# Kernel optimization log

Hardware: AMD Instinct MI355X
Metric: run time of the kernel (lower is better)

## Reference

```python
import jax, jax.numpy as jnp
import numpy as np
from jax import lax

NUM_GROUP = 512
GROUP_SIZE = 32


def setup_inputs() -> dict:
    key = jax.random.key(0)
    xyz = jax.random.normal(key, (8, 8192, 6), dtype=jnp.float32)
    return {"xyz": xyz}


def _fps_indices(pts, K):
    """Farthest point sampling. pts: [B,N,3] -> idx [B,K] int32. Start at point 0."""
    B, N, _ = pts.shape
    first = jnp.zeros((B,), dtype=jnp.int32)
    # squared distance of every point to the first selected point
    d = jnp.sum((pts - pts[:, :1, :]) ** 2, axis=-1)  # [B,N]

    def step(d, _):
        nxt = jnp.argmax(d, axis=1).astype(jnp.int32)              # [B]
        newp = jnp.take_along_axis(pts, nxt[:, None, None], axis=1)  # [B,1,3]
        d = jnp.minimum(d, jnp.sum((pts - newp) ** 2, axis=-1))
        return d, nxt

    _, rest = lax.scan(step, d, None, length=K - 1)  # rest: [K-1,B]
    idx = jnp.concatenate([first[None, :], rest], axis=0)  # [K,B]
    return idx.T  # [B,K]


def _group(xyz, num_group, group_size):
    coords = xyz[:, :, :3]    # [B,N,3]
    normals = xyz[:, :, 3:6]  # [B,N,3]

    fps_idx = _fps_indices(coords, num_group)                          # [B,G]
    center = jnp.take_along_axis(coords, fps_idx[:, :, None], axis=1)  # [B,G,3]

    # pairwise squared distances center->points: [B,G,N]
    c2 = jnp.sum(center ** 2, axis=-1)[:, :, None]
    x2 = jnp.sum(coords ** 2, axis=-1)[:, None, :]
    cx = jnp.einsum('bgd,bnd->bgn', center, coords)
    d2 = c2 - 2.0 * cx + x2

    _, knn_idx = lax.top_k(-d2, group_size)  # [B,G,M] nearest neighbors

    flat_idx = knn_idx.reshape(knn_idx.shape[0], -1)  # [B,G*M]
    neigh = jnp.take_along_axis(coords, flat_idx[:, :, None], axis=1)
    neigh = neigh.reshape(-1, num_group, group_size, 3) - center[:, :, None, :]
    neigh_n = jnp.take_along_axis(normals, flat_idx[:, :, None], axis=1)
    neigh_n = neigh_n.reshape(-1, num_group, group_size, 3)
    return neigh, neigh_n, center


def reference(xyz):
    return _group(xyz, NUM_GROUP, GROUP_SIZE)
```

## Files before the change

### kernel.cpp

```cpp
#include <hip/hip_runtime.h>
#include <stdint.h>

#define BATCH 8
#define NPTS 8192
#define NGRP 512
#define GSZ 32

typedef float vf2 __attribute__((ext_vector_type(2)));

__device__ __forceinline__ float sq3(float dx, float dy, float dz) {
    return __fadd_rn(__fadd_rn(__fmul_rn(dx, dx), __fmul_rn(dy, dy)), __fmul_rn(dz, dz));
}

template <int C>
__device__ __forceinline__ float dpp_max_f32_step(float v) {
    const int t = __builtin_amdgcn_update_dpp(__float_as_int(v), __float_as_int(v),
                                              C, 0xF, 0xF, false);
    return fmaxf(v, __int_as_float(t));
}
template <int C>
__device__ __forceinline__ unsigned dpp_min_u32_step(unsigned v) {
    const unsigned t = (unsigned)__builtin_amdgcn_update_dpp((int)v, (int)v,
                                                             C, 0xF, 0xF, false);
    return v < t ? v : t;
}
__device__ __forceinline__ float wave_max_f32(float v) {
    v = dpp_max_f32_step<0x111>(v);
    v = dpp_max_f32_step<0x112>(v);
    v = dpp_max_f32_step<0x114>(v);
    v = dpp_max_f32_step<0x118>(v);
    v = dpp_max_f32_step<0x142>(v);
    v = dpp_max_f32_step<0x143>(v);
    return __int_as_float(__builtin_amdgcn_readlane(__float_as_int(v), 63));
}
__device__ __forceinline__ unsigned wave_min_u32(unsigned v) {
    v = dpp_min_u32_step<0x111>(v);
    v = dpp_min_u32_step<0x112>(v);
    v = dpp_min_u32_step<0x114>(v);
    v = dpp_min_u32_step<0x118>(v);
    v = dpp_min_u32_step<0x142>(v);
    v = dpp_min_u32_step<0x143>(v);
    return (unsigned)__builtin_amdgcn_readlane((int)v, 63);
}

__global__ __launch_bounds__(512) void fps_kernel(const float* __restrict__ xyz,
                                                  float* __restrict__ centers) {
    const int b = blockIdx.x;
    const int tid = threadIdx.x;
    const int wv = tid >> 6;

    __shared__ float4 P4[NPTS];
    __shared__ double pkey[2][8];
    __shared__ float cl[NGRP * 3];

    vf2 px[8], py[8], pz[8], d2[8];
    const float* base = xyz + (size_t)b * NPTS * 6;

#pragma unroll
    for (int i = 0; i < 16; ++i) {
        const int p = i * 512 + tid;
        const float4 v4 = *reinterpret_cast<const float4*>(base + (size_t)p * 6);
        px[i >> 1][i & 1] = v4.x; py[i >> 1][i & 1] = v4.y; pz[i >> 1][i & 1] = v4.z;
        d2[i >> 1][i & 1] = __int_as_float(0x7f800000);
        P4[p] = make_float4(v4.x, v4.y, v4.z, 0.0f);
    }
    float Bx = base[0], By = base[1], Bz = base[2];
    if (tid == 0) { cl[0] = Bx; cl[1] = By; cl[2] = Bz; }
    __syncthreads();

    for (int k = 1; k < NGRP; ++k) {
        {
#pragma clang fp contract(off)
            const vf2 bx2 = {Bx, Bx}, by2 = {By, By}, bz2 = {Bz, Bz};
#pragma unroll
            for (int j = 0; j < 8; ++j) {
                const vf2 dx = px[j] - bx2;
                const vf2 dy = py[j] - by2;
                const vf2 dz = pz[j] - bz2;
                const vf2 mx2 = dx * dx;
                const vf2 my2 = dy * dy;
                const vf2 mz2 = dz * dz;
                const vf2 s = (mx2 + my2) + mz2;
                d2[j] = __builtin_elementwise_min(d2[j], s);
            }
        }
        vf2 mv = d2[0];
#pragma unroll
        for (int j = 1; j < 8; ++j) mv = __builtin_elementwise_max(mv, d2[j]);
        const float mx = fmaxf(mv[0], mv[1]);
        const float wmx = wave_max_f32(mx);
        int wi = 0;
#pragma unroll
        for (int i = 15; i >= 1; --i) {
            wi = (d2[i >> 1][i & 1] == mx) ? i : wi;
        }
        unsigned widx_w;
        const unsigned long long bal = __ballot(mx == wmx);
        if (__popcll(bal) == 1) {
            const int L = __ffsll(bal) - 1;
            widx_w = (unsigned)(__builtin_amdgcn_readlane(wi, L) * 512 + (wv * 64 + L));
        } else {
            const unsigned cand = (mx == wmx) ? (unsigned)(wi * 512 + tid) : 0xFFFFFFFFu;
            widx_w = wave_min_u32(cand);
        }

        const int buf = k & 1;
        if ((tid & 63) == 0) {
            pkey[buf][wv] = __hiloint2double(__float_as_int(wmx), 8191 - (int)widx_w);
        }
        __syncthreads();

        const double2* pp = reinterpret_cast<const double2*>(&pkey[buf][0]);
        const double2 a = pp[0], c = pp[1], e = pp[2], f = pp[3];
        const double g = fmax(fmax(fmax(a.x, a.y), fmax(c.x, c.y)),
                              fmax(fmax(e.x, e.y), fmax(f.x, f.y)));
        const int widx = 8191 - __double2loint(g);
        const float4 c4 = P4[widx];
        Bx = c4.x; By = c4.y; Bz = c4.z;

        if (tid == 0) { cl[k * 3 + 0] = Bx; cl[k * 3 + 1] = By; cl[k * 3 + 2] = Bz; }
    }

    __syncthreads();
    float* cg = centers + (size_t)b * NGRP * 3;
    for (int t = tid; t < NGRP * 3; t += 512) cg[t] = cl[t];
}

__global__ __launch_bounds__(256) void knn_kernel(const float* __restrict__ xyz,
                                                  const float* __restrict__ centers,
                                                  float* __restrict__ neigh,
                                                  float* __restrict__ neigh_n) {
    const int row = blockIdx.x;
    const int b = row >> 9;
    const int tid = threadIdx.x;
    const int lane = tid & 63;
    const int wv = tid >> 6;

    __shared__ unsigned long long rk[2][4];
    __shared__ int sel[GSZ];

    const float* cptr = centers + (size_t)row * 3;
    const float cx = cptr[0], cy = cptr[1], cz = cptr[2];
    const float c2 = sq3(cx, cy, cz);

    const float* base = xyz + (size_t)b * NPTS * 6;
    unsigned long long key[32];
#pragma unroll
    for (int i = 0; i < 32; ++i) {
        const int p = i * 256 + tid;
        const float4 v4 = *reinterpret_cast<const float4*>(base + (size_t)p * 6);
        const float x = v4.x, y = v4.y, z = v4.z;
        const float x2 = sq3(x, y, z);
        const float dot = __fmaf_rn(cz, z, __fmaf_rn(cy, y, __fmul_rn(cx, x)));
        const float d2 = __fadd_rn(__fsub_rn(c2, __fmul_rn(2.0f, dot)), x2);
        unsigned u = __float_as_uint(d2);
        u ^= (unsigned)(((int)u >> 31)) | 0x80000000u;
        key[i] = ((unsigned long long)u << 32) | (unsigned)p;
    }

    unsigned long long lm = ~0ULL, lm2v = ~0ULL;
#pragma unroll
    for (int i = 0; i < 32; ++i) {
        const unsigned long long kk = key[i];
        const bool a = kk < lm;
        const bool b2 = kk < lm2v;
        lm2v = a ? lm : (b2 ? kk : lm2v);
        lm = a ? kk : lm;
    }

    for (int r = 0; r < GSZ; ++r) {
        const unsigned hi = (unsigned)(lm >> 32);
        const unsigned minhi = wave_min_u32(hi);
        unsigned minlo;
        const unsigned long long bal = __ballot(hi == minhi);
        if (__popcll(bal) == 1) {
            const int L = __ffsll(bal) - 1;
            minlo = (unsigned)__builtin_amdgcn_readlane((int)(unsigned)lm, L);
        } else {
            const unsigned cand = (hi == minhi) ? (unsigned)lm : 0xFFFFFFFFu;
            minlo = wave_min_u32(cand);
        }
        const unsigned long long mk = ((unsigned long long)minhi << 32) | minlo;

        const int rb = r & 1;
        if (lane == 0) rk[rb][wv] = mk;
        __syncthreads();
        const ulonglong2* rp = reinterpret_cast<const ulonglong2*>(&rk[rb][0]);
        const ulonglong2 r0 = rp[0], r1 = rp[1];
        const unsigned long long g01 = r0.x < r0.y ? r0.x : r0.y;
        const unsigned long long g23 = r1.x < r1.y ? r1.x : r1.y;
        const unsigned long long gm = g01 < g23 ? g01 : g23;
        if (tid == 0) sel[r] = (int)(unsigned)(gm & 0xffffffffu);
        if (lm == gm) {
            if (lm2v != 0ULL) {
                lm = lm2v;
            } else {
                unsigned long long nm = ~0ULL;
#pragma unroll
                for (int i = 0; i < 32; ++i) {
                    const unsigned long long v = key[i] > gm ? key[i] : ~0ULL;
                    nm = v < nm ? v : nm;
                }
                lm = nm;
            }
            lm2v = 0ULL;
        }
    }
    __syncthreads();

    if (tid < GSZ) {
        const int idx = sel[tid];
        const float* q = base + (size_t)idx * 6;
        const float4 a4 = *reinterpret_cast<const float4*>(q);
        const float2 b2v = *reinterpret_cast<const float2*>(q + 4);
        const size_t o = ((size_t)row * GSZ + tid) * 3;
        neigh[o + 0] = __fsub_rn(a4.x, cx);
        neigh[o + 1] = __fsub_rn(a4.y, cy);
        neigh[o + 2] = __fsub_rn(a4.z, cz);
        neigh_n[o + 0] = a4.w;
        neigh_n[o + 1] = b2v.x;
        neigh_n[o + 2] = b2v.y;
    }
}

extern "C" void kernel_launch(void* const* d_in, const int* in_sizes, int n_in,
                              void* d_out, int out_size, void* d_ws, size_t ws_size,
                              hipStream_t stream) {
    const float* xyz = (const float*)d_in[0];
    float* out = (float*)d_out;
    float* neigh   = out;
    float* neigh_n = out + (size_t)BATCH * NGRP * GSZ * 3;
    float* centers = out + (size_t)2 * BATCH * NGRP * GSZ * 3;

    fps_kernel<<<BATCH, 512, 0, stream>>>(xyz, centers);
    knn_kernel<<<BATCH * NGRP, 256, 0, stream>>>(xyz, centers, neigh, neigh_n);
}
```

Baseline: 511.9 us.

## Fuse FPS and KNN into a persistent kernel with flag-based streaming of centers

Merges the FPS and KNN kernels into one launch. Eight blocks run farthest point sampling and publish centers in chunks of 16 through workspace arrays and a per-batch release counter. The remaining 248 worker blocks spin on that counter and run KNN for each center as soon as it is available, so KNN overlaps the serial FPS instead of waiting for it to finish. KNN blocks grow to 512 threads with 16 keys per thread. The change relies on all FPS blocks being co-resident with the spinning workers and adds a small zeroing kernel; the workers' spinning and memory traffic may slow the FPS blocks.

After: 547.9 us. +7.0%, slower.

```diff
diff --git a/kernel.cpp b/kernel.cpp
--- a/kernel.cpp
+++ b/kernel.cpp
@@ -5,7 +5,9 @@
 #define NPTS 8192
 #define NGRP 512
 #define GSZ 32
-
+#define NWORK 248
+#define CHUNK 16
+typedef unsigned long long u64;
 typedef float vf2 __attribute__((ext_vector_type(2)));
 
 __device__ __forceinline__ float sq3(float dx, float dy, float dz) {
@@ -43,183 +45,225 @@
     return (unsigned)__builtin_amdgcn_readlane((int)v, 63);
 }
 
-__global__ __launch_bounds__(512) void fps_kernel(const float* __restrict__ xyz,
-                                                  float* __restrict__ centers) {
-    const int b = blockIdx.x;
-    const int tid = threadIdx.x;
-    const int wv = tid >> 6;
-
+__global__ void zero_rc(unsigned* __restrict__ rc) {
+    if (threadIdx.x < BATCH) rc[threadIdx.x] = 0;
+}
+
+__global__ __launch_bounds__(512) void fused_kernel(const float* __restrict__ xyz,
+                                                    float* __restrict__ centers,
+                                                    float* __restrict__ neigh,
+                                                    float* __restrict__ neigh_n,
+                                                    unsigned* __restrict__ rc,
+                                                    unsigned* __restrict__ cpx,
+                                                    unsigned* __restrict__ cpy,
+                                                    unsigned* __restrict__ cpz) {
     __shared__ float4 P4[NPTS];
     __shared__ double pkey[2][8];
     __shared__ float cl[NGRP * 3];
-
-    vf2 px[8], py[8], pz[8], d2[8];
-    const float* base = xyz + (size_t)b * NPTS * 6;
-
-#pragma unroll
-    for (int i = 0; i < 16; ++i) {
-        const int p = i * 512 + tid;
-        const float4 v4 = *reinterpret_cast<const float4*>(base + (size_t)p * 6);
-        px[i >> 1][i & 1] = v4.x; py[i >> 1][i & 1] = v4.y; pz[i >> 1][i & 1] = v4.z;
-        d2[i >> 1][i & 1] = __int_as_float(0x7f800000);
-        P4[p] = make_float4(v4.x, v4.y, v4.z, 0.0f);
-    }
-    float Bx = base[0], By = base[1], Bz = base[2];
-    if (tid == 0) { cl[0] = Bx; cl[1] = By; cl[2] = Bz; }
-    __syncthreads();
-
-    for (int k = 1; k < NGRP; ++k) {
-        {
-#pragma clang fp contract(off)
-            const vf2 bx2 = {Bx, Bx}, by2 = {By, By}, bz2 = {Bz, Bz};
-#pragma unroll
-            for (int j = 0; j < 8; ++j) {
-                const vf2 dx = px[j] - bx2;
-                const vf2 dy = py[j] - by2;
-                const vf2 dz = pz[j] - bz2;
-                const vf2 mx2 = dx * dx;
-                const vf2 my2 = dy * dy;
-                const vf2 mz2 = dz * dz;
-                const vf2 s = (mx2 + my2) + mz2;
-                d2[j] = __builtin_elementwise_min(d2[j], s);
-            }
-        }
-        vf2 mv = d2[0];
-#pragma unroll
-        for (int j = 1; j < 8; ++j) mv = __builtin_elementwise_max(mv, d2[j]);
-        const float mx = fmaxf(mv[0], mv[1]);
-        const float wmx = wave_max_f32(mx);
-        int wi = 0;
-#pragma unroll
-        for (int i = 15; i >= 1; --i) {
-            wi = (d2[i >> 1][i & 1] == mx) ? i : wi;
-        }
-        unsigned widx_w;
-        const unsigned long long bal = __ballot(mx == wmx);
-        if (__popcll(bal) == 1) {
-            const int L = __ffsll(bal) - 1;
-            widx_w = (unsigned)(__builtin_amdgcn_readlane(wi, L) * 512 + (wv * 64 + L));
-        } else {
-            const unsigned cand = (mx == wmx) ? (unsigned)(wi * 512 + tid) : 0xFFFFFFFFu;
-            widx_w = wave_min_u32(cand);
-        }
-
-        const int buf = k & 1;
-        if ((tid & 63) == 0) {
-            pkey[buf][wv] = __hiloint2double(__float_as_int(wmx), 8191 - (int)widx_w);
-        }
-        __syncthreads();
-
-        const double2* pp = reinterpret_cast<const double2*>(&pkey[buf][0]);
-        const double2 a = pp[0], c = pp[1], e = pp[2], f = pp[3];
-        const double g = fmax(fmax(fmax(a.x, a.y), fmax(c.x, c.y)),
-                              fmax(fmax(e.x, e.y), fmax(f.x, f.y)));
-        const int widx = 8191 - __double2loint(g);
-        const float4 c4 = P4[widx];
-        Bx = c4.x; By = c4.y; Bz = c4.z;
-
-        if (tid == 0) { cl[k * 3 + 0] = Bx; cl[k * 3 + 1] = By; cl[k * 3 + 2] = Bz; }
-    }
-
-    __syncthreads();
-    float* cg = centers + (size_t)b * NGRP * 3;
-    for (int t = tid; t < NGRP * 3; t += 512) cg[t] = cl[t];
-}
-
-__global__ __launch_bounds__(256) void knn_kernel(const float* __restrict__ xyz,
-                                                  const float* __restrict__ centers,
-                                                  float* __restrict__ neigh,
-                                                  float* __restrict__ neigh_n) {
-    const int row = blockIdx.x;
-    const int b = row >> 9;
+    __shared__ u64 rk[2][8];
+    __shared__ int sel[GSZ];
+
+    const int wid = blockIdx.x;
     const int tid = threadIdx.x;
     const int lane = tid & 63;
     const int wv = tid >> 6;
 
-    __shared__ unsigned long long rk[2][4];
-    __shared__ int sel[GSZ];
-
-    const float* cptr = centers + (size_t)row * 3;
-    const float cx = cptr[0], cy = cptr[1], cz = cptr[2];
-    const float c2 = sq3(cx, cy, cz);
-
-    const float* base = xyz + (size_t)b * NPTS * 6;
-    unsigned long long key[32];
-#pragma unroll
-    for (int i = 0; i < 32; ++i) {
-        const int p = i * 256 + tid;
-        const float4 v4 = *reinterpret_cast<const float4*>(base + (size_t)p * 6);
-        const float x = v4.x, y = v4.y, z = v4.z;
-        const float x2 = sq3(x, y, z);
-        const float dot = __fmaf_rn(cz, z, __fmaf_rn(cy, y, __fmul_rn(cx, x)));
-        const float d2 = __fadd_rn(__fsub_rn(c2, __fmul_rn(2.0f, dot)), x2);
-        unsigned u = __float_as_uint(d2);
-        u ^= (unsigned)(((int)u >> 31)) | 0x80000000u;
-        key[i] = ((unsigned long long)u << 32) | (unsigned)p;
-    }
-
-    unsigned long long lm = ~0ULL, lm2v = ~0ULL;
-#pragma unroll
-    for (int i = 0; i < 32; ++i) {
-        const unsigned long long kk = key[i];
-        const bool a = kk < lm;
-        const bool b2 = kk < lm2v;
-        lm2v = a ? lm : (b2 ? kk : lm2v);
-        lm = a ? kk : lm;
-    }
-
-    for (int r = 0; r < GSZ; ++r) {
-        const unsigned hi = (unsigned)(lm >> 32);
-        const unsigned minhi = wave_min_u32(hi);
-        unsigned minlo;
-        const unsigned long long bal = __ballot(hi == minhi);
-        if (__popcll(bal) == 1) {
-            const int L = __ffsll(bal) - 1;
-            minlo = (unsigned)__builtin_amdgcn_readlane((int)(unsigned)lm, L);
-        } else {
-            const unsigned cand = (hi == minhi) ? (unsigned)lm : 0xFFFFFFFFu;
-            minlo = wave_min_u32(cand);
+    if (wid < BATCH) {
+        const int b = wid;
+        vf2 px[8], py[8], pz[8], d2[8];
+        const float* base = xyz + (size_t)b * NPTS * 6;
+
+#pragma unroll
+        for (int i = 0; i < 16; ++i) {
+            const int p = i * 512 + tid;
+            const float4 v4 = *reinterpret_cast<const float4*>(base + (size_t)p * 6);
+            px[i >> 1][i & 1] = v4.x; py[i >> 1][i & 1] = v4.y; pz[i >> 1][i & 1] = v4.z;
+            d2[i >> 1][i & 1] = __int_as_float(0x7f800000);
+            P4[p] = make_float4(v4.x, v4.y, v4.z, 0.0f);
         }
-        const unsigned long long mk = ((unsigned long long)minhi << 32) | minlo;
-
-        const int rb = r & 1;
-        if (lane == 0) rk[rb][wv] = mk;
+        float Bx = base[0], By = base[1], Bz = base[2];
+        if (tid == 0) { cl[0] = Bx; cl[1] = By; cl[2] = Bz; }
         __syncthreads();
-        const ulonglong2* rp = reinterpret_cast<const ulonglong2*>(&rk[rb][0]);
-        const ulonglong2 r0 = rp[0], r1 = rp[1];
-        const unsigned long long g01 = r0.x < r0.y ? r0.x : r0.y;
-        const unsigned long long g23 = r1.x < r1.y ? r1.x : r1.y;
-        const unsigned long long gm = g01 < g23 ? g01 : g23;
-        if (tid == 0) sel[r] = (int)(unsigned)(gm & 0xffffffffu);
-        if (lm == gm) {
-            if (lm2v != 0ULL) {
-                lm = lm2v;
+
+        for (int k = 1; k < NGRP; ++k) {
+            {
+#pragma clang fp contract(off)
+                const vf2 bx2 = {Bx, Bx}, by2 = {By, By}, bz2 = {Bz, Bz};
+#pragma unroll
+                for (int j = 0; j < 8; ++j) {
+                    const vf2 dx = px[j] - bx2;
+                    const vf2 dy = py[j] - by2;
+                    const vf2 dz = pz[j] - bz2;
+                    const vf2 mx2 = dx * dx;
+                    const vf2 my2 = dy * dy;
+                    const vf2 mz2 = dz * dz;
+                    const vf2 s = (mx2 + my2) + mz2;
+                    d2[j] = __builtin_elementwise_min(d2[j], s);
+                }
+            }
+            vf2 mv = d2[0];
+#pragma unroll
+            for (int j = 1; j < 8; ++j) mv = __builtin_elementwise_max(mv, d2[j]);
+            const float mx = fmaxf(mv[0], mv[1]);
+            const float wmx = wave_max_f32(mx);
+            int wi = 0;
+#pragma unroll
+            for (int i = 15; i >= 1; --i) {
+                wi = (d2[i >> 1][i & 1] == mx) ? i : wi;
+            }
+            unsigned widx_w;
+            const u64 bal = __ballot(mx == wmx);
+            if (__popcll(bal) == 1) {
+                const int L = __ffsll(bal) - 1;
+                widx_w = (unsigned)(__builtin_amdgcn_readlane(wi, L) * 512 + (wv * 64 + L));
             } else {
-                unsigned long long nm = ~0ULL;
-#pragma unroll
-                for (int i = 0; i < 32; ++i) {
-                    const unsigned long long v = key[i] > gm ? key[i] : ~0ULL;
-                    nm = v < nm ? v : nm;
-                }
-                lm = nm;
-            }
-            lm2v = 0ULL;
+                const unsigned cand = (mx == wmx) ? (unsigned)(wi * 512 + tid) : 0xFFFFFFFFu;
+                widx_w = wave_min_u32(cand);
+            }
+
+            const int buf = k & 1;
+            if ((tid & 63) == 0) {
+                pkey[buf][wv] = __hiloint2double(__float_as_int(wmx), 8191 - (int)widx_w);
+            }
+            __syncthreads();
+
+            const double2* pp = reinterpret_cast<const double2*>(&pkey[buf][0]);
+            const double2 a = pp[0], c = pp[1], e = pp[2], f = pp[3];
+            const double g = fmax(fmax(fmax(a.x, a.y), fmax(c.x, c.y)),
+                                  fmax(fmax(e.x, e.y), fmax(f.x, f.y)));
+            const int widx = 8191 - __double2loint(g);
+            const float4 c4 = P4[widx];
+            Bx = c4.x; By = c4.y; Bz = c4.z;
+
+            if (tid == 0) {
+                cl[k * 3 + 0] = Bx; cl[k * 3 + 1] = By; cl[k * 3 + 2] = Bz;
+                if ((k & (CHUNK - 1)) == (CHUNK - 1)) {
+                    const int k0 = k - (CHUNK - 1);
+#pragma unroll
+                    for (int j = 0; j < CHUNK; ++j) {
+                        const int kk = k0 + j;
+                        const int gi = b * NGRP + kk;
+                        __hip_atomic_store(&cpx[gi], __float_as_uint(cl[kk * 3 + 0]),
+                                           __ATOMIC_RELAXED, __HIP_MEMORY_SCOPE_AGENT);
+                        __hip_atomic_store(&cpy[gi], __float_as_uint(cl[kk * 3 + 1]),
+                                           __ATOMIC_RELAXED, __HIP_MEMORY_SCOPE_AGENT);
+                        __hip_atomic_store(&cpz[gi], __float_as_uint(cl[kk * 3 + 2]),
+                                           __ATOMIC_RELAXED, __HIP_MEMORY_SCOPE_AGENT);
+                    }
+                    __hip_atomic_store(&rc[b], (unsigned)(k + 1),
+                                       __ATOMIC_RELEASE, __HIP_MEMORY_SCOPE_AGENT);
+                }
+            }
         }
-    }
-    __syncthreads();
-
-    if (tid < GSZ) {
-        const int idx = sel[tid];
-        const float* q = base + (size_t)idx * 6;
-        const float4 a4 = *reinterpret_cast<const float4*>(q);
-        const float2 b2v = *reinterpret_cast<const float2*>(q + 4);
-        const size_t o = ((size_t)row * GSZ + tid) * 3;
-        neigh[o + 0] = __fsub_rn(a4.x, cx);
-        neigh[o + 1] = __fsub_rn(a4.y, cy);
-        neigh[o + 2] = __fsub_rn(a4.z, cz);
-        neigh_n[o + 0] = a4.w;
-        neigh_n[o + 1] = b2v.x;
-        neigh_n[o + 2] = b2v.y;
+
+        __syncthreads();
+        float* cg = centers + (size_t)b * NGRP * 3;
+        for (int t = tid; t < NGRP * 3; t += 512) cg[t] = cl[t];
+
+    } else {
+        for (int t = wid - BATCH; t < BATCH * NGRP; t += NWORK) {
+            const int b = t & 7, g = t >> 3;
+            if (tid == 0) {
+                while (__hip_atomic_load(&rc[b], __ATOMIC_ACQUIRE,
+                                         __HIP_MEMORY_SCOPE_AGENT) <= (unsigned)g) {
+                    __builtin_amdgcn_s_sleep(2);
+                }
+            }
+            __syncthreads();
+
+            const int gi = b * NGRP + g;
+            const float cx = __uint_as_float(__hip_atomic_load(
+                &cpx[gi], __ATOMIC_RELAXED, __HIP_MEMORY_SCOPE_AGENT));
+            const float cy = __uint_as_float(__hip_atomic_load(
+                &cpy[gi], __ATOMIC_RELAXED, __HIP_MEMORY_SCOPE_AGENT));
+            const float cz = __uint_as_float(__hip_atomic_load(
+                &cpz[gi], __ATOMIC_RELAXED, __HIP_MEMORY_SCOPE_AGENT));
+            const float c2 = sq3(cx, cy, cz);
+
+            const float* base = xyz + (size_t)b * NPTS * 6;
+            u64 key[16];
+#pragma unroll
+            for (int i = 0; i < 16; ++i) {
+                const int p = i * 512 + tid;
+                const float4 v4 = *reinterpret_cast<const float4*>(base + (size_t)p * 6);
+                const float x = v4.x, y = v4.y, z = v4.z;
+                const float x2 = sq3(x, y, z);
+                const float dot = __fmaf_rn(cz, z, __fmaf_rn(cy, y, __fmul_rn(cx, x)));
+                const float dd = __fadd_rn(__fsub_rn(c2, __fmul_rn(2.0f, dot)), x2);
+                unsigned u = __float_as_uint(dd);
+                u ^= (unsigned)(((int)u >> 31)) | 0x80000000u;
+                key[i] = ((u64)u << 32) | (unsigned)p;
+            }
+
+            u64 lm = ~0ULL, lm2v = ~0ULL;
+#pragma unroll
+            for (int i = 0; i < 16; ++i) {
+                const u64 kk = key[i];
+                const bool a = kk < lm;
+                const bool b2 = kk < lm2v;
+                lm2v = a ? lm : (b2 ? kk : lm2v);
+                lm = a ? kk : lm;
+            }
+
+            for (int r = 0; r < GSZ; ++r) {
+                const unsigned hi = (unsigned)(lm >> 32);
+                const unsigned minhi = wave_min_u32(hi);
+                unsigned minlo;
+                const u64 bal = __ballot(hi == minhi);
+                if (__popcll(bal) == 1) {
+                    const int L = __ffsll(bal) - 1;
+                    minlo = (unsigned)__builtin_amdgcn_readlane((int)(unsigned)lm, L);
+                } else {
+                    const unsigned cand = (hi == minhi) ? (unsigned)lm : 0xFFFFFFFFu;
+                    minlo = wave_min_u32(cand);
+                }
+                const u64 mk = ((u64)minhi << 32) | minlo;
+
+                const int rb = r & 1;
+                if (lane == 0) rk[rb][wv] = mk;
+                __syncthreads();
+                const ulonglong2* rp = reinterpret_cast<const ulonglong2*>(&rk[rb][0]);
+                const ulonglong2 r0 = rp[0], r1 = rp[1], r2 = rp[2], r3 = rp[3];
+                const u64 m0 = r0.x < r0.y ? r0.x : r0.y;
+                const u64 m1 = r1.x < r1.y ? r1.x : r1.y;
+                const u64 m2 = r2.x < r2.y ? r2.x : r2.y;
+                const u64 m3 = r3.x < r3.y ? r3.x : r3.y;
+                const u64 m01 = m0 < m1 ? m0 : m1;
+                const u64 m23 = m2 < m3 ? m2 : m3;
+                const u64 gm = m01 < m23 ? m01 : m23;
+                if (tid == 0) sel[r] = (int)(unsigned)(gm & 0xffffffffu);
+                if (lm == gm) {
+                    if (lm2v != 0ULL) {
+                        lm = lm2v;
+                    } else {
+                        u64 nm = ~0ULL;
+#pragma unroll
+                        for (int i = 0; i < 16; ++i) {
+                            const u64 v = key[i] > gm ? key[i] : ~0ULL;
+                            nm = v < nm ? v : nm;
+                        }
+                        lm = nm;
+                    }
+                    lm2v = 0ULL;
+                }
+            }
+            __syncthreads();
+
+            if (tid < GSZ) {
+                const int idx = sel[tid];
+                const float* q = base + (size_t)idx * 6;
+                const float4 a4 = *reinterpret_cast<const float4*>(q);
+                const float2 b2v = *reinterpret_cast<const float2*>(q + 4);
+                const int row = b * NGRP + g;
+                const size_t o = ((size_t)row * GSZ + tid) * 3;
+                neigh[o + 0] = __fsub_rn(a4.x, cx);
+                neigh[o + 1] = __fsub_rn(a4.y, cy);
+                neigh[o + 2] = __fsub_rn(a4.z, cz);
+                neigh_n[o + 0] = a4.w;
+                neigh_n[o + 1] = b2v.x;
+                neigh_n[o + 2] = b2v.y;
+            }
+        }
     }
 }
 
@@ -232,6 +276,12 @@
     float* neigh_n = out + (size_t)BATCH * NGRP * GSZ * 3;
     float* centers = out + (size_t)2 * BATCH * NGRP * GSZ * 3;
 
-    fps_kernel<<<BATCH, 512, 0, stream>>>(xyz, centers);
-    knn_kernel<<<BATCH * NGRP, 256, 0, stream>>>(xyz, centers, neigh, neigh_n);
-}
+    unsigned* rc  = (unsigned*)d_ws;
+    unsigned* cpx = (unsigned*)((char*)d_ws + 1024);
+    unsigned* cpy = (unsigned*)((char*)d_ws + 1024 + 16384);
+    unsigned* cpz = (unsigned*)((char*)d_ws + 1024 + 32768);
+
+    zero_rc<<<1, 64, 0, stream>>>(rc);
+    fused_kernel<<<BATCH + NWORK, 512, 0, stream>>>(xyz, centers, neigh, neigh_n,
+                                                    rc, cpx, cpy, cpz);
+}
```

## Select per-wave top-32 in KNN without block barriers, then merge in one wave

Applied to the files above, without the earlier changes.

Each of the four waves in the KNN kernel now pops its own 32 smallest distance keys independently and writes them to shared memory, with no block-wide barrier per round. Wave 0 then merges the 128 candidates with 32 more wave-level min reductions. This removes the 32 per-round __syncthreads and shared-memory exchanges. The cost is an extra serial merge phase on one wave and some redundant per-wave pops beyond the global top 32.

Result: slower. 533.7 us (+4.3%).

```diff
diff --git a/kernel.cpp b/kernel.cpp
--- a/kernel.cpp
+++ b/kernel.cpp
@@ -5,7 +5,7 @@
 #define NPTS 8192
 #define NGRP 512
 #define GSZ 32
-
+typedef unsigned long long u64;
 typedef float vf2 __attribute__((ext_vector_type(2)));
 
 __device__ __forceinline__ float sq3(float dx, float dy, float dz) {
@@ -41,6 +41,20 @@
     v = dpp_min_u32_step<0x142>(v);
     v = dpp_min_u32_step<0x143>(v);
     return (unsigned)__builtin_amdgcn_readlane((int)v, 63);
+}
+__device__ __forceinline__ u64 wave_min_u64(u64 lm) {
+    const unsigned hi = (unsigned)(lm >> 32);
+    const unsigned minhi = wave_min_u32(hi);
+    unsigned minlo;
+    const u64 bal = __ballot(hi == minhi);
+    if (__popcll(bal) == 1) {
+        const int L = __ffsll(bal) - 1;
+        minlo = (unsigned)__builtin_amdgcn_readlane((int)(unsigned)lm, L);
+    } else {
+        const unsigned cand = (hi == minhi) ? (unsigned)lm : 0xFFFFFFFFu;
+        minlo = wave_min_u32(cand);
+    }
+    return ((u64)minhi << 32) | minlo;
 }
 
 __global__ __launch_bounds__(512) void fps_kernel(const float* __restrict__ xyz,
@@ -95,7 +109,7 @@
             wi = (d2[i >> 1][i & 1] == mx) ? i : wi;
         }
         unsigned widx_w;
-        const unsigned long long bal = __ballot(mx == wmx);
+        const u64 bal = __ballot(mx == wmx);
         if (__popcll(bal) == 1) {
             const int L = __ffsll(bal) - 1;
             widx_w = (unsigned)(__builtin_amdgcn_readlane(wi, L) * 512 + (wv * 64 + L));
@@ -136,7 +150,7 @@
     const int lane = tid & 63;
     const int wv = tid >> 6;
 
-    __shared__ unsigned long long rk[2][4];
+    __shared__ u64 wl[4][GSZ];
     __shared__ int sel[GSZ];
 
     const float* cptr = centers + (size_t)row * 3;
@@ -144,7 +158,7 @@
     const float c2 = sq3(cx, cy, cz);
 
     const float* base = xyz + (size_t)b * NPTS * 6;
-    unsigned long long key[32];
+    u64 key[32];
 #pragma unroll
     for (int i = 0; i < 32; ++i) {
         const int p = i * 256 + tid;
@@ -155,13 +169,13 @@
         const float d2 = __fadd_rn(__fsub_rn(c2, __fmul_rn(2.0f, dot)), x2);
         unsigned u = __float_as_uint(d2);
         u ^= (unsigned)(((int)u >> 31)) | 0x80000000u;
-        key[i] = ((unsigned long long)u << 32) | (unsigned)p;
-    }
-
-    unsigned long long lm = ~0ULL, lm2v = ~0ULL;
+        key[i] = ((u64)u << 32) | (unsigned)p;
+    }
+
+    u64 lm = ~0ULL, lm2v = ~0ULL;
 #pragma unroll
     for (int i = 0; i < 32; ++i) {
-        const unsigned long long kk = key[i];
+        const u64 kk = key[i];
         const bool a = kk < lm;
         const bool b2 = kk < lm2v;
         lm2v = a ? lm : (b2 ? kk : lm2v);
@@ -169,41 +183,35 @@
     }
 
     for (int r = 0; r < GSZ; ++r) {
-        const unsigned hi = (unsigned)(lm >> 32);
-        const unsigned minhi = wave_min_u32(hi);
-        unsigned minlo;
-        const unsigned long long bal = __ballot(hi == minhi);
-        if (__popcll(bal) == 1) {
-            const int L = __ffsll(bal) - 1;
-            minlo = (unsigned)__builtin_amdgcn_readlane((int)(unsigned)lm, L);
-        } else {
-            const unsigned cand = (hi == minhi) ? (unsigned)lm : 0xFFFFFFFFu;
-            minlo = wave_min_u32(cand);
-        }
-        const unsigned long long mk = ((unsigned long long)minhi << 32) | minlo;
-
-        const int rb = r & 1;
-        if (lane == 0) rk[rb][wv] = mk;
-        __syncthreads();
-        const ulonglong2* rp = reinterpret_cast<const ulonglong2*>(&rk[rb][0]);
-        const ulonglong2 r0 = rp[0], r1 = rp[1];
-        const unsigned long long g01 = r0.x < r0.y ? r0.x : r0.y;
-        const unsigned long long g23 = r1.x < r1.y ? r1.x : r1.y;
-        const unsigned long long gm = g01 < g23 ? g01 : g23;
-        if (tid == 0) sel[r] = (int)(unsigned)(gm & 0xffffffffu);
-        if (lm == gm) {
+        const u64 mk = wave_min_u64(lm);
+        if (lane == 0) wl[wv][r] = mk;
+        if (lm == mk) {
             if (lm2v != 0ULL) {
                 lm = lm2v;
             } else {
-                unsigned long long nm = ~0ULL;
+                u64 nm = ~0ULL;
 #pragma unroll
                 for (int i = 0; i < 32; ++i) {
-                    const unsigned long long v = key[i] > gm ? key[i] : ~0ULL;
+                    const u64 v = key[i] > mk ? key[i] : ~0ULL;
                     nm = v < nm ? v : nm;
                 }
                 lm = nm;
             }
             lm2v = 0ULL;
+        }
+    }
+    __syncthreads();
+
+    if (wv == 0) {
+        u64 c0 = wl[lane >> 5][lane & 31];
+        u64 c1 = wl[2 + (lane >> 5)][lane & 31];
+        for (int r = 0; r < GSZ; ++r) {
+            const u64 m = c0 < c1 ? c0 : c1;
+            const u64 gm = wave_min_u64(m);
+            if (lane == 0) sel[r] = (int)(unsigned)gm;
+            if (m == gm) {
+                if (c0 == gm) c0 = ~0ULL; else c1 = ~0ULL;
+            }
         }
     }
     __syncthreads();
```
